# Performance work log

Measured on AMD Instinct MI355X. Metric: run time of the kernel, lower is better.

## Reference

```python
import jax, jax.numpy as jnp
import numpy as np

T_ENC = 80
MAX_LEN = 80
B = 64
D_IN = 4096
EU = 1024
DU = 1024
VOCAB = 20000
ATT = 80


def _lstm_scan(xs, h0, c0, W_ih, W_hh, b_ih, b_hh):
    """Single-layer LSTM over leading time dim. xs: [T,B,I]. Returns (ys[T,B,H], hT, cT)."""
    def step(carry, x):
        h, c = carry
        g = x @ W_ih.T + b_ih + h @ W_hh.T + b_hh
        i, f, gg, o = jnp.split(g, 4, axis=-1)
        c = jax.nn.sigmoid(f) * c + jax.nn.sigmoid(i) * jnp.tanh(gg)
        h = jax.nn.sigmoid(o) * jnp.tanh(c)
        return (h, c), h
    (hT, cT), ys = jax.lax.scan(step, (h0, c0), xs)
    return ys, hT, cT


def setup_inputs() -> dict:
    key = jax.random.key(0)
    ks = jax.random.split(key, 20)
    s = 0.05
    inp = {
        "input_data": jax.random.normal(ks[0], (T_ENC, B, D_IN), jnp.float32),
        "correct_answer": jax.random.normal(ks[1], (MAX_LEN, B, VOCAB), jnp.float32),
        # encoder LSTM params (torch gate order i,f,g,o)
        "enc_W_ih": jax.random.normal(ks[2], (4 * EU, D_IN), jnp.float32) * s,
        "enc_W_hh": jax.random.normal(ks[3], (4 * EU, EU), jnp.float32) * s,
        "enc_b_ih": jax.random.normal(ks[4], (4 * EU,), jnp.float32) * s,
        "enc_b_hh": jax.random.normal(ks[5], (4 * EU,), jnp.float32) * s,
        # decoder LSTM: input = decoder_unit + encoder_unit
        "dec_W_ih": jax.random.normal(ks[6], (4 * DU, DU + EU), jnp.float32) * s,
        "dec_W_hh": jax.random.normal(ks[7], (4 * DU, DU), jnp.float32) * s,
        "dec_b_ih": jax.random.normal(ks[8], (4 * DU,), jnp.float32) * s,
        "dec_b_hh": jax.random.normal(ks[9], (4 * DU,), jnp.float32) * s,
        # embeddings
        "in_emb_W": jax.random.normal(ks[10], (DU, VOCAB), jnp.float32) * s,
        "in_emb_b": jax.random.normal(ks[11], (DU,), jnp.float32) * s,
        "out_emb_W": jax.random.normal(ks[12], (VOCAB, DU), jnp.float32) * s,
        "out_emb_b": jax.random.normal(ks[13], (VOCAB,), jnp.float32) * s,
        # attention: linear_l1du_max ((d_l+1)*d_u -> 80), linear_2du_du (2*d_u -> d_u)
        "att_W1": jax.random.normal(ks[14], (ATT, 2 * DU), jnp.float32) * s,
        "att_b1": jax.random.normal(ks[15], (ATT,), jnp.float32) * s,
        "att_W2": jax.random.normal(ks[16], (DU, 2 * DU), jnp.float32) * s,
        "att_b2": jax.random.normal(ks[17], (DU,), jnp.float32) * s,
        "prelu_w": jnp.full((1,), 0.25, jnp.float32),  # PReLU(num_parameters=1) init
        "max_len": 80,
        "real_ans_length": jax.random.randint(ks[18], (B,), 0, 80),
    }
    return inp


def reference(input_data, correct_answer,
              enc_W_ih, enc_W_hh, enc_b_ih, enc_b_hh,
              dec_W_ih, dec_W_hh, dec_b_ih, dec_b_hh,
              in_emb_W, in_emb_b, out_emb_W, out_emb_b,
              att_W1, att_b1, att_W2, att_b2, prelu_w,
              max_len, real_ans_length):
    z_eh = jnp.zeros((B, EU), jnp.float32)
    z_dh = jnp.zeros((B, DU), jnp.float32)

    # encoding stage
    enc_seq, enc_h, enc_c = _lstm_scan(input_data, z_eh, z_eh, enc_W_ih, enc_W_hh, enc_b_ih, enc_b_hh)
    pad_tag = jnp.zeros((input_data.shape[0], B, DU), jnp.float32)
    dec_in0 = jnp.concatenate([enc_seq, pad_tag], axis=2)
    dec_out_seq, dec_h, dec_c = _lstm_scan(dec_in0, z_dh, z_dh, dec_W_ih, dec_W_hh, dec_b_ih, dec_b_hh)

    # encoder over zero padding inputs (continues encoder state)
    pad_in = jnp.zeros((max_len, B, D_IN), jnp.float32)
    enc_pad_seq, _, _ = _lstm_scan(pad_in, enc_h, enc_c, enc_W_ih, enc_W_hh, enc_b_ih, enc_b_hh)

    # teacher-forced samples (schedule_sample_rate == 1 -> always ground truth)
    bos = jnp.zeros((B, VOCAB), jnp.float32).at[:, -2].set(1.0)
    sample0 = bos @ in_emb_W.T + in_emb_b                              # [B, DU]
    samples_rest = correct_answer[1:max_len] @ in_emb_W.T + in_emb_b  # [max_len-1, B, DU]
    samples = jnp.concatenate([sample0[None], samples_rest], axis=0)   # [max_len, B, DU]

    E = enc_seq  # [80, B, EU]; attention weights have exactly 80 slots

    def dec_step(carry, inp):
        h, c = carry
        sample, enc_pad = inp
        # Attention: i = h (single layer), a = concat(i, word)
        a = jnp.concatenate([h, sample], axis=-1)          # [B, 2*DU]
        w = jax.nn.softmax(a @ att_W1.T + att_b1, axis=1)  # [B, 80]
        f = jnp.einsum('bs,sbh->bh', w, E)                 # [B, EU]
        cc = jnp.concatenate([sample, f], axis=-1)         # [B, 2*DU]
        z = cc @ att_W2.T + att_b2
        o = jnp.where(z >= 0, z, prelu_w[0] * z)           # PReLU (scalar param)
        context = o + enc_pad                              # [B, EU]
        x = jnp.concatenate([sample, context], axis=-1)    # [B, DU+EU]
        g = x @ dec_W_ih.T + dec_b_ih + h @ dec_W_hh.T + dec_b_hh
        gi, gf, gg, go = jnp.split(g, 4, axis=-1)
        c = jax.nn.sigmoid(gf) * c + jax.nn.sigmoid(gi) * jnp.tanh(gg)
        h = jax.nn.sigmoid(go) * jnp.tanh(c)
        word = h @ out_emb_W.T + out_emb_b                 # [B, VOCAB]
        return (h, c), word

    (_, _), words = jax.lax.scan(dec_step, (dec_h, dec_c), (samples, enc_pad_seq))
    return words  # [max_len, B, VOCAB]
```

## Files before the change

### kernel.cpp

```cpp
#include <hip/hip_runtime.h>
#include <cstddef>
#include <cstdint>

typedef __attribute__((ext_vector_type(8))) short short8v;
typedef __attribute__((ext_vector_type(4))) float f32x4;

__device__ __forceinline__ float sigmf(float x) { return 1.0f / (1.0f + __expf(-x)); }

__device__ __forceinline__ unsigned short bf16_rn(float x) {
    union { float f; unsigned u; } v; v.f = x;
    unsigned r = v.u + 0x7FFF + ((v.u >> 16) & 1);
    return (unsigned short)(r >> 16);
}
__device__ __forceinline__ float bf16_to_f(unsigned short h) {
    union { unsigned u; float f; } v; v.u = ((unsigned)h) << 16; return v.f;
}
__device__ __forceinline__ unsigned long long pack4(unsigned short a, unsigned short b,
                                                    unsigned short c, unsigned short d) {
    return (unsigned long long)a | ((unsigned long long)b << 16)
         | ((unsigned long long)c << 32) | ((unsigned long long)d << 48);
}

#define MFMA_(d, va, vb) d = __builtin_amdgcn_mfma_f32_16x16x32_bf16(va, vb, d, 0, 0, 0)

#define AT_LD(p)        __hip_atomic_load((p), __ATOMIC_RELAXED, __HIP_MEMORY_SCOPE_AGENT)
#define AT_ST(p, v)     __hip_atomic_store((p), (v), __ATOMIC_RELAXED, __HIP_MEMORY_SCOPE_AGENT)
#define AT_ST_REL(p, v) __hip_atomic_store((p), (v), __ATOMIC_RELEASE, __HIP_MEMORY_SCOPE_AGENT)
#define AT_ADD(p, v)    __hip_atomic_fetch_add((p), (v), __ATOMIC_RELAXED, __HIP_MEMORY_SCOPE_AGENT)

__device__ __forceinline__ void write_frag3_nt(unsigned short* __restrict__ dst, int NRGW,
                                               int r, int k, float x)
{
    unsigned short hi = bf16_rn(x); float r1 = x - bf16_to_f(hi);
    unsigned short md = bf16_rn(r1);
    unsigned short lo = bf16_rn(r1 - bf16_to_f(md));
    int base = (((r >> 4) * 32 + (k >> 5)) * 64 + ((k >> 3) & 3) * 16 + (r & 15)) * 8 + (k & 7);
    int ps = NRGW * 16384;
    __builtin_nontemporal_store(hi, &dst[base]);
    __builtin_nontemporal_store(md, &dst[ps + base]);
    __builtin_nontemporal_store(lo, &dst[2 * ps + base]);
}

__launch_bounds__(256)
__global__ void rearr_frag(const float* __restrict__ src, int ld, int c0,
                           unsigned short* __restrict__ dst, int R, int K)
{
    int idx = blockIdx.x * 256 + threadIdx.x;
    int kpr = K >> 3;
    if (idx >= R * kpr) return;
    int r = idx / kpr, k = (idx % kpr) * 8;
    int NRGW = R >> 4;
    const float* s = src + (size_t)r * ld + c0 + k;
    float4 v0 = *(const float4*)s, v1 = *(const float4*)(s + 4);
    float xs[8] = {v0.x, v0.y, v0.z, v0.w, v1.x, v1.y, v1.z, v1.w};
    unsigned short hi[8], md[8], lo[8];
#pragma unroll
    for (int e = 0; e < 8; ++e) {
        hi[e] = bf16_rn(xs[e]); float r1 = xs[e] - bf16_to_f(hi[e]);
        md[e] = bf16_rn(r1);
        lo[e] = bf16_rn(r1 - bf16_to_f(md[e]));
    }
    int base = (((r >> 4) * 32 + (k >> 5)) * 64 + ((k >> 3) & 3) * 16 + (r & 15)) * 8;
    size_t ps = (size_t)NRGW * 16384;
    *(unsigned long long*)&dst[base]          = pack4(hi[0], hi[1], hi[2], hi[3]);
    *(unsigned long long*)&dst[base + 4]      = pack4(hi[4], hi[5], hi[6], hi[7]);
    *(unsigned long long*)&dst[ps + base]     = pack4(md[0], md[1], md[2], md[3]);
    *(unsigned long long*)&dst[ps + base + 4] = pack4(md[4], md[5], md[6], md[7]);
    *(unsigned long long*)&dst[2*ps + base]     = pack4(lo[0], lo[1], lo[2], lo[3]);
    *(unsigned long long*)&dst[2*ps + base + 4] = pack4(lo[4], lo[5], lo[6], lo[7]);
}

__device__ __forceinline__ void tree_barrier(unsigned* bar, int gidx, int ng, int bpg)
{
    __syncthreads();
    if (threadIdx.x == 0) {
        unsigned* gcnt = bar + gidx * 32;
        unsigned* ggen = bar + gidx * 32 + 1;
        unsigned* rcnt = bar + ng * 32;
        unsigned* rgen = bar + ng * 32 + 1;
        __threadfence();
        unsigned mygen = AT_LD(ggen);
        unsigned prev = AT_ADD(gcnt, 1u);
        if (prev == (unsigned)(bpg - 1)) {
            AT_ST(gcnt, 0u);
            unsigned rg = AT_LD(rgen);
            unsigned rprev = AT_ADD(rcnt, 1u);
            if (rprev == (unsigned)(ng - 1)) {
                AT_ST(rcnt, 0u);
                AT_ST_REL(rgen, rg + 1u);
            } else {
                while (AT_LD(rgen) == rg) __builtin_amdgcn_s_sleep(1);
            }
            AT_ST_REL(ggen, mygen + 1u);
        } else {
            while (AT_LD(ggen) == mygen) __builtin_amdgcn_s_sleep(1);
        }
        __threadfence();
    }
    __syncthreads();
}

template <int NS>
__launch_bounds__(256, 2)
__global__ void gemm_mfma_split(const float* __restrict__ A, int lda,
                                const float* __restrict__ W, int ldw,
                                float* __restrict__ C, int ldc,
                                const float* __restrict__ bias,
                                int M, int N, int K)
{
    __shared__ unsigned short Abf[NS][128][40];
    __shared__ unsigned short Bbf[NS][128][40];
    const int tid = threadIdx.x;
    const int m0 = blockIdx.y * 128, n0 = blockIdx.x * 128;
    const int wave = tid >> 6, lane = tid & 63;
    const int wr = wave >> 1, wc = wave & 1;
    const int lr = lane & 15, lk = (lane >> 4) * 8;

    f32x4 acc[4][4];
#pragma unroll
    for (int i = 0; i < 4; ++i)
#pragma unroll
        for (int j = 0; j < 4; ++j) acc[i][j] = (f32x4){0.f, 0.f, 0.f, 0.f};

    const int arow = tid >> 1;
    const int akh  = (tid & 1) * 16;
    int gr = m0 + arow; if (gr > M - 1) gr = M - 1;
    int gn = n0 + arow; if (gn > N - 1) gn = N - 1;
    const float* aptr = A + (size_t)gr * lda + akh;
    const float* wptr = W + (size_t)gn * ldw + akh;

    for (int k0 = 0; k0 < K; k0 += 32) {
#pragma unroll
        for (int q = 0; q < 4; ++q) {
            float4 v = *(const float4*)(aptr + k0 + q * 4);
            float xs[4] = {v.x, v.y, v.z, v.w};
            unsigned short h[4], hm[4], hl[4];
#pragma unroll
            for (int e = 0; e < 4; ++e) {
                h[e] = bf16_rn(xs[e]);
                if (NS == 3) {
                    float r1 = xs[e] - bf16_to_f(h[e]);
                    hm[e] = bf16_rn(r1);
                    hl[e] = bf16_rn(r1 - bf16_to_f(hm[e]));
                }
            }
            *(unsigned long long*)&Abf[0][arow][akh + q * 4] = pack4(h[0], h[1], h[2], h[3]);
            if (NS == 3) {
                *(unsigned long long*)&Abf[1][arow][akh + q * 4] = pack4(hm[0], hm[1], hm[2], hm[3]);
                *(unsigned long long*)&Abf[2][arow][akh + q * 4] = pack4(hl[0], hl[1], hl[2], hl[3]);
            }
        }
#pragma unroll
        for (int q = 0; q < 4; ++q) {
            float4 v = *(const float4*)(wptr + k0 + q * 4);
            float xs[4] = {v.x, v.y, v.z, v.w};
            unsigned short h[4], hm[4], hl[4];
#pragma unroll
            for (int e = 0; e < 4; ++e) {
                h[e] = bf16_rn(xs[e]);
                if (NS == 3) {
                    float r1 = xs[e] - bf16_to_f(h[e]);
                    hm[e] = bf16_rn(r1);
                    hl[e] = bf16_rn(r1 - bf16_to_f(hm[e]));
                }
            }
            *(unsigned long long*)&Bbf[0][arow][akh + q * 4] = pack4(h[0], h[1], h[2], h[3]);
            if (NS == 3) {
                *(unsigned long long*)&Bbf[1][arow][akh + q * 4] = pack4(hm[0], hm[1], hm[2], hm[3]);
                *(unsigned long long*)&Bbf[2][arow][akh + q * 4] = pack4(hl[0], hl[1], hl[2], hl[3]);
            }
        }
        __syncthreads();

        short8v a[NS][4], b[4];
#pragma unroll
        for (int p = 0; p < NS; ++p)
#pragma unroll
            for (int i = 0; i < 4; ++i)
                a[p][i] = *(const short8v*)&Abf[p][wr * 64 + i * 16 + lr][lk];
#pragma unroll
        for (int q = 0; q < NS; ++q) {
#pragma unroll
            for (int j = 0; j < 4; ++j)
                b[j] = *(const short8v*)&Bbf[q][wc * 64 + j * 16 + lr][lk];
            const int pmax = (NS == 1) ? 1 : (3 - q);
#pragma unroll
            for (int p = 0; p < 3; ++p) {
                if (p >= pmax) break;
#pragma unroll
                for (int i = 0; i < 4; ++i)
#pragma unroll
                    for (int j = 0; j < 4; ++j)
                        acc[i][j] = __builtin_amdgcn_mfma_f32_16x16x32_bf16(
                            a[p][i], b[j], acc[i][j], 0, 0, 0);
            }
        }
        __syncthreads();
    }

    const int crow = (lane >> 4) * 4;
#pragma unroll
    for (int i = 0; i < 4; ++i) {
        int mbase = m0 + wr * 64 + i * 16 + crow;
#pragma unroll
        for (int j = 0; j < 4; ++j) {
            int n = n0 + wc * 64 + j * 16 + lr;
            if (n < N) {
                float bv = bias[n];
#pragma unroll
                for (int r = 0; r < 4; ++r) {
                    int m = mbase + r;
                    if (m < M) C[(size_t)m * ldc + n] = acc[i][j][r] + bv;
                }
            }
        }
    }
}

__launch_bounds__(256)
__global__ void zero_f(float* __restrict__ p, int n)
{
    int i = blockIdx.x * 256 + threadIdx.x;
    if (i < n) p[i] = 0.f;
}

__launch_bounds__(256)
__global__ void vec_add2(const float* __restrict__ a, const float* __restrict__ b,
                         float* __restrict__ o, int n)
{
    int i = blockIdx.x * 256 + threadIdx.x;
    if (i < n) o[i] = a[i] + b[i];
}

__launch_bounds__(256)
__global__ void sample0_fill(const float* __restrict__ emW, const float* __restrict__ emb,
                             float* __restrict__ samples)
{
    int idx = blockIdx.x * 256 + threadIdx.x;
    int d = idx & 1023;
    samples[idx] = emW[(size_t)d * 20000 + 19998] + emb[d];
}

__device__ __forceinline__ void stage_A(unsigned short* __restrict__ LDSA,
                                        const unsigned short* __restrict__ src,
                                        int rg, int tid)
{
#pragma unroll
    for (int p = 0; p < 3; ++p) {
        const unsigned short* sp = src + (size_t)(p * 4 + rg) * 16384;
        unsigned short* dp = LDSA + p * 16384;
#pragma unroll
        for (int it = 0; it < 4; ++it) {
            int idx = tid + it * 512;
            *(short8v*)&dp[idx * 8] = *(const short8v*)&sp[idx * 8];
        }
    }
}

__device__ __forceinline__ f32x4 mfma16(const unsigned short* __restrict__ LDSA,
                                        const short8v* __restrict__ wreg,
                                        int kh, int lane)
{
    f32x4 acc0 = (f32x4){0.f,0.f,0.f,0.f}, acc1 = acc0;
#pragma unroll
    for (int i = 0; i < 16; ++i) {
        int kf = kh * 16 + i;
        short8v a0 = *(const short8v*)&LDSA[(kf * 64 + lane) * 8];
        short8v a1 = *(const short8v*)&LDSA[16384 + (kf * 64 + lane) * 8];
        short8v a2 = *(const short8v*)&LDSA[32768 + (kf * 64 + lane) * 8];
        short8v b0 = wreg[i * 3 + 0], b1 = wreg[i * 3 + 1], b2 = wreg[i * 3 + 2];
        f32x4& A = (i & 1) ? acc1 : acc0;
        MFMA_(A, a0, b0); MFMA_(A, a0, b1); MFMA_(A, a1, b0);
        MFMA_(A, a1, b1); MFMA_(A, a0, b2); MFMA_(A, a2, b0);
    }
    return acc0 + acc1;
}

__launch_bounds__(512, 1)
__attribute__((amdgpu_waves_per_eu(1, 2)))
__global__ void coop_enc80(const unsigned short* __restrict__ WencF,
                           const float* __restrict__ Xbig,
                           unsigned short* __restrict__ hfrag,
                           float* __restrict__ enc_seq,
                           float* __restrict__ cglobE,
                           unsigned* __restrict__ bar)
{
    __shared__ unsigned short LDSA[3 * 16384];
    __shared__ float gbuf[8][16][16];
    const int bid = blockIdx.x, tid = threadIdx.x;
    const int w = tid >> 6, lane = tid & 63;
    const int g = w & 3, kh = w >> 2;
    const int rg = bid & 3, cg = bid >> 2;
    const int wbase = g * 64 + cg;
    const int r_l = (tid & 255) >> 4, c_l = tid & 15;
    const int row = rg * 16 + r_l, col = cg * 16 + c_l;
    float cstate = 0.f;

    short8v wreg[48];
#pragma unroll
    for (int i = 0; i < 16; ++i) {
        int kf = kh * 16 + i;
#pragma unroll
        for (int p = 0; p < 3; ++p)
            wreg[i * 3 + p] = *(const short8v*)&WencF[((size_t)(p * 256 + wbase) * 32 + kf) * 512 + lane * 8];
    }

    float pf[4];
    if (tid < 256) {
#pragma unroll
        for (int g2 = 0; g2 < 4; ++g2)
            pf[g2] = Xbig[(size_t)row * 4096 + g2 * 1024 + col];
    }

    for (int s = 0; s < 80; ++s) {
        const unsigned short* hf = hfrag + (s & 1) * 196608;
        stage_A(LDSA, hf, rg, tid);
        __syncthreads();
        f32x4 acc = mfma16(LDSA, wreg, kh, lane);
#pragma unroll
        for (int r = 0; r < 4; ++r)
            gbuf[w][(lane >> 4) * 4 + r][lane & 15] = acc[r];
        __syncthreads();

        if (tid < 256) {
            float gv[4];
#pragma unroll
            for (int g2 = 0; g2 < 4; ++g2)
                gv[g2] = gbuf[g2][r_l][c_l] + gbuf[4 + g2][r_l][c_l] + pf[g2];
            float cn = sigmf(gv[1]) * cstate + sigmf(gv[0]) * tanhf(gv[2]);
            float hn = sigmf(gv[3]) * tanhf(cn);
            cstate = cn;
            __builtin_nontemporal_store(hn, &enc_seq[(size_t)s * 65536 + row * 1024 + col]);
            write_frag3_nt(hfrag + ((s + 1) & 1) * 196608, 4, row, col, hn);
            if (s == 79) __builtin_nontemporal_store(cstate, &cglobE[row * 1024 + col]);
            else {
#pragma unroll
                for (int g2 = 0; g2 < 4; ++g2)
                    pf[g2] = Xbig[((size_t)(s + 1) * 64 + row) * 4096 + g2 * 1024 + col];
            }
        }
        tree_barrier(bar, bid >> 5, 8, 32);
    }
}

__launch_bounds__(512, 1)
__attribute__((amdgpu_waves_per_eu(1, 2)))
__global__ void coop_padwarm(const unsigned short* __restrict__ WencF,
                             const unsigned short* __restrict__ WdecF,
                             const float* __restrict__ benc,
                             const float* __restrict__ Xwarm,
                             const float* __restrict__ cglobE,
                             unsigned short* __restrict__ hfragE,
                             unsigned short* __restrict__ hfragD,
                             float* __restrict__ enc_pad,
                             float* __restrict__ cglobD,
                             float* __restrict__ h_fp32,
                             unsigned* __restrict__ barE,
                             unsigned* __restrict__ barW)
{
    __shared__ unsigned short LDSA[3 * 16384];
    __shared__ float gbuf[8][16][16];
    const int bid = blockIdx.x, tid = threadIdx.x;
    const int w = tid >> 6, lane = tid & 63;
    const int g = w & 3, kh = w >> 2;
    const bool isW = bid >= 128;
    const int lb = bid & 127;
    const int rg2 = lb & 1, cg = lb >> 1;
    const int wbase = g * 64 + cg;
    const int r_l = (tid & 255) >> 4, c_l = tid & 15;
    const int col = cg * 16 + c_l;
    const unsigned short* Wf = isW ? WdecF : WencF;
    unsigned short* hfrag = isW ? hfragD : hfragE;
    unsigned* bar = isW ? barW : barE;

    short8v wreg[48];
#pragma unroll
    for (int i = 0; i < 16; ++i) {
        int kf = kh * 16 + i;
#pragma unroll
        for (int p = 0; p < 3; ++p)
            wreg[i * 3 + p] = *(const short8v*)&Wf[((size_t)(p * 256 + wbase) * 32 + kf) * 512 + lane * 8];
    }

    float cst[2] = {0.f, 0.f};
    float pfx[2][4];
    if (tid < 256) {
#pragma unroll
        for (int l = 0; l < 2; ++l) {
            int row = rg2 * 32 + l * 16 + r_l;
            if (!isW) cst[l] = cglobE[row * 1024 + col];
#pragma unroll
            for (int g2 = 0; g2 < 4; ++g2)
                pfx[l][g2] = isW ? Xwarm[(size_t)row * 4096 + g2 * 1024 + col]
                                 : benc[g2 * 1024 + col];
        }
    }

    for (int s = 0; s < 80; ++s) {
        const unsigned short* hf = hfrag + (s & 1) * 196608;
        unsigned short* hout = hfrag + ((s + 1) & 1) * 196608;
#pragma unroll
        for (int l = 0; l < 2; ++l) {
            const int rgi = rg2 * 2 + l;
            stage_A(LDSA, hf, rgi, tid);
            __syncthreads();
            f32x4 acc = mfma16(LDSA, wreg, kh, lane);
#pragma unroll
            for (int r = 0; r < 4; ++r)
                gbuf[w][(lane >> 4) * 4 + r][lane & 15] = acc[r];
            __syncthreads();
            if (tid < 256) {
                const int row = rgi * 16 + r_l;
                float gv[4];
#pragma unroll
                for (int g2 = 0; g2 < 4; ++g2)
                    gv[g2] = gbuf[g2][r_l][c_l] + gbuf[4 + g2][r_l][c_l] + pfx[l][g2];
                float cn = sigmf(gv[1]) * cst[l] + sigmf(gv[0]) * tanhf(gv[2]);
                float hn = sigmf(gv[3]) * tanhf(cn);
                cst[l] = cn;
                if (!isW)
                    __builtin_nontemporal_store(hn, &enc_pad[(size_t)s * 65536 + row * 1024 + col]);
                write_frag3_nt(hout, 4, row, col, hn);
                if (isW) {
                    if (s == 79) {
                        __builtin_nontemporal_store(hn, &h_fp32[row * 1024 + col]);
                        __builtin_nontemporal_store(cn, &cglobD[row * 1024 + col]);
                    } else {
#pragma unroll
                        for (int g2 = 0; g2 < 4; ++g2)
                            pfx[l][g2] = Xwarm[((size_t)(s + 1) * 64 + row) * 4096 + g2 * 1024 + col];
                    }
                }
            }
            __syncthreads();
        }
        tree_barrier(bar, (lb >> 5), 4, 32);
    }
}

__launch_bounds__(512, 2)
__global__ void coop_dec80(const unsigned short* __restrict__ WihcF,
                           const unsigned short* __restrict__ WhhF,
                           const float* __restrict__ W1,
                           const float* __restrict__ EW2,
                           const float* __restrict__ S_g,
                           const float* __restrict__ ctxS,
                           const float* __restrict__ S_log,
                           const float* __restrict__ enc_pad,
                           const float* __restrict__ prelu_w,
                           const float* __restrict__ h_fp32,
                           const float* __restrict__ cglobD,
                           unsigned short* __restrict__ hfrag,
                           unsigned short* __restrict__ ctxfrag,
                           float* __restrict__ plog,
                           float* __restrict__ h_all,
                           float* __restrict__ gsum,
                           unsigned* __restrict__ bar)
{
    __shared__ float EW2T[80 * 256];
    __shared__ float gred[8][1024];
    __shared__ float hq[256];
    __shared__ float wsm[80];
    __shared__ float rbuf[128];
    const int bid = blockIdx.x, tid = threadIdx.x;
    const int w = tid >> 6, lane = tid & 63;
    const int gg = bid >> 6, cg = bid & 63;
    const int wbase = gg * 64 + cg;
    const int kq = w;
    const int b = bid >> 2, jc = bid & 3;
    const float pw = prelu_w[0];

    const unsigned short* Wsrc = (kq < 4) ? WihcF : WhhF;
    const int kfbase = (kq & 3) * 8;
    short8v wreg[24];
#pragma unroll
    for (int i = 0; i < 8; ++i) {
#pragma unroll
        for (int p = 0; p < 3; ++p)
            wreg[i * 3 + p] = *(const short8v*)&Wsrc[((size_t)(p * 256 + wbase) * 32 + kfbase + i) * 512 + lane * 8];
    }

    float cstate = (tid < 256) ? cglobD[b * 1024 + jc * 256 + tid] : 0.f;

    for (int i = tid; i < 80 * 256; i += 512) {
        int ss = i >> 8, j = i & 255;
        EW2T[i] = EW2[((size_t)ss * 64 + b) * 1024 + jc * 256 + j];
    }
    __syncthreads();

    for (int s = 80; s < 160; ++s) {
        unsigned short* hout = hfrag + ((s + 1) & 1) * 196608;
        const unsigned short* hf = hfrag + (s & 1) * 196608;
        const int t = s - 80;

        if (s == 80) {
            float* hsm_ = (float*)gred;
            for (int i = tid; i < 1024; i += 512) hsm_[i] = h_fp32[b * 1024 + i];
            __syncthreads();
#pragma unroll
            for (int i = 0; i < 10; ++i) {
                int sx = w * 10 + i;
                float p = 0.f;
#pragma unroll
                for (int q = 0; q < 16; ++q)
                    p = fmaf(hsm_[lane + q * 64], W1[(size_t)sx * 2048 + lane + q * 64], p);
#pragma unroll
                for (int off = 32; off; off >>= 1) p += __shfl_down(p, off, 64);
                if (lane == 0) wsm[sx] = p + S_log[((size_t)t * 64 + b) * 80 + sx];
            }
            __syncthreads();
        } else {
            if (tid < 80) {
                float l4 = plog[(b * 4 + 0) * 80 + tid] + plog[(b * 4 + 1) * 80 + tid]
                         + plog[(b * 4 + 2) * 80 + tid] + plog[(b * 4 + 3) * 80 + tid];
                wsm[tid] = l4 + S_log[((size_t)t * 64 + b) * 80 + tid];
            }
            __syncthreads();
        }
        float v = (tid < 80) ? wsm[tid] : -3.4e38f;
        if (tid < 128) rbuf[tid] = v;
        __syncthreads();
        for (int off = 64; off >= 1; off >>= 1) {
            if (tid < off) rbuf[tid] = fmaxf(rbuf[tid], rbuf[tid + off]);
            __syncthreads();
        }
        float mx = rbuf[0];
        __syncthreads();
        float e = (tid < 80) ? __expf(wsm[tid] - mx) : 0.f;
        if (tid < 128) rbuf[tid] = e;
        __syncthreads();
        for (int off = 64; off >= 1; off >>= 1) {
            if (tid < off) rbuf[tid] += rbuf[tid + off];
            __syncthreads();
        }
        float inv = 1.f / rbuf[0];
        __syncthreads();
        if (tid < 80) wsm[tid] = e * inv;
        __syncthreads();
        if (tid < 256) {
            float f = 0.f;
#pragma unroll 8
            for (int ss = 0; ss < 80; ++ss)
                f = fmaf(wsm[ss], EW2T[ss * 256 + tid], f);
            int col = jc * 256 + tid;
            float val = f + ctxS[((size_t)t * 64 + b) * 1024 + col];
            val = (val >= 0.f) ? val : pw * val;
            val += enc_pad[((size_t)t * 64 + b) * 1024 + col];
            write_frag3_nt(ctxfrag, 4, b, col, val);
        }
        tree_barrier(bar, bid >> 5, 8, 32);

        float pf[4];
        if (tid < 256) {
            const float* xb = S_g + ((size_t)t * 64 + b) * 4096;
            int col = jc * 256 + tid;
#pragma unroll
            for (int g2 = 0; g2 < 4; ++g2) pf[g2] = xb[g2 * 1024 + col];
        }

        {
            f32x4 acc[4];
#pragma unroll
            for (int rg = 0; rg < 4; ++rg) acc[rg] = (f32x4){0.f,0.f,0.f,0.f};
            const unsigned short* asrc = (kq < 4) ? ctxfrag : hf;
#pragma unroll
            for (int i = 0; i < 8; ++i) {
                int kfl = kfbase + i;
#pragma unroll
                for (int rg = 0; rg < 4; ++rg) {
                    const unsigned short* ab = asrc + ((size_t)rg * 32 + kfl) * 512 + lane * 8;
                    short8v a0 = *(const short8v*)&ab[0];
                    short8v a1 = *(const short8v*)&ab[65536];
                    short8v a2 = *(const short8v*)&ab[131072];
                    short8v b0 = wreg[i * 3 + 0], b1 = wreg[i * 3 + 1], b2 = wreg[i * 3 + 2];
                    MFMA_(acc[rg], a0, b0); MFMA_(acc[rg], a0, b1); MFMA_(acc[rg], a1, b0);
                    MFMA_(acc[rg], a1, b1); MFMA_(acc[rg], a0, b2); MFMA_(acc[rg], a2, b0);
                }
            }
#pragma unroll
            for (int rg = 0; rg < 4; ++rg)
#pragma unroll
                for (int r = 0; r < 4; ++r)
                    gred[w][rg * 256 + lane * 4 + r] = acc[rg][r];
            __syncthreads();
#pragma unroll
            for (int e2 = 0; e2 < 2; ++e2) {
                int slot = tid * 2 + e2;
                int rg = slot >> 8, l = (slot >> 2) & 63, r = slot & 3;
                float sum = 0.f;
#pragma unroll
                for (int w2 = 0; w2 < 8; ++w2) sum += gred[w2][slot];
                int row = rg * 16 + (l >> 4) * 4 + r;
                int col = cg * 16 + (l & 15);
                __builtin_nontemporal_store(sum, &gsum[((size_t)gg * 64 + row) * 1024 + col]);
            }
        }
        tree_barrier(bar, bid >> 5, 8, 32);

        if (tid < 256) {
            int col = jc * 256 + tid;
            float gv[4];
#pragma unroll
            for (int g2 = 0; g2 < 4; ++g2)
                gv[g2] = gsum[((size_t)g2 * 64 + b) * 1024 + col] + pf[g2];
            float cn = sigmf(gv[1]) * cstate + sigmf(gv[0]) * tanhf(gv[2]);
            float hn = sigmf(gv[3]) * tanhf(cn);
            cstate = cn;
            __builtin_nontemporal_store(hn, &h_all[((size_t)t * 64 + b) * 1024 + col]);
            write_frag3_nt(hout, 4, b, col, hn);
            hq[tid] = hn;
        }
        __syncthreads();
        if (s < 159) {
#pragma unroll
            for (int i = 0; i < 10; ++i) {
                int sx = w * 10 + i;
                float p = 0.f;
#pragma unroll
                for (int q = 0; q < 4; ++q)
                    p = fmaf(hq[lane + q * 64], W1[(size_t)sx * 2048 + jc * 256 + lane + q * 64], p);
#pragma unroll
                for (int off = 32; off; off >>= 1) p += __shfl_down(p, off, 64);
                if (lane == 0) __builtin_nontemporal_store(p, &plog[(b * 4 + jc) * 80 + sx]);
            }
        }
        tree_barrier(bar, bid >> 5, 8, 32);
    }
}

extern "C" void kernel_launch(void* const* d_in, const int* in_sizes, int n_in,
                              void* d_out, int out_size, void* d_ws, size_t ws_size,
                              hipStream_t stream)
{
    (void)in_sizes; (void)n_in; (void)out_size; (void)ws_size;

    const float* input_data     = (const float*)d_in[0];
    const float* correct_answer = (const float*)d_in[1];
    const float* enc_W_ih = (const float*)d_in[2];
    const float* enc_W_hh = (const float*)d_in[3];
    const float* enc_b_ih = (const float*)d_in[4];
    const float* enc_b_hh = (const float*)d_in[5];
    const float* dec_W_ih = (const float*)d_in[6];
    const float* dec_W_hh = (const float*)d_in[7];
    const float* dec_b_ih = (const float*)d_in[8];
    const float* dec_b_hh = (const float*)d_in[9];
    const float* in_emb_W = (const float*)d_in[10];
    const float* in_emb_b = (const float*)d_in[11];
    const float* out_emb_W = (const float*)d_in[12];
    const float* out_emb_b = (const float*)d_in[13];
    const float* att_W1 = (const float*)d_in[14];
    const float* att_b1 = (const float*)d_in[15];
    const float* att_W2 = (const float*)d_in[16];
    const float* att_b2 = (const float*)d_in[17];
    const float* prelu_w = (const float*)d_in[18];

    float* out = (float*)d_out;
    char* ws = (char*)d_ws;

    float* Xbig    = out;
    float* S_g     = out + 20971520;
    float* ctxS    = out + 41943040;
    float* S_log   = out + 47185920;
    float* samples = out + 47595520;
    float* EW2     = out + 52838400;
    unsigned short* WencF = (unsigned short*)(out + 58081280);
    unsigned short* WhhDF = (unsigned short*)(out + 64372736);
    unsigned short* WihcF = (unsigned short*)(out + 70664192);

    size_t off = 0;
    auto alloc = [&](size_t nfloats) { float* p = (float*)(ws + off); off += nfloats * 4; return p; };
    float* enc_seq = alloc(80 * 64 * 1024);
    float* enc_pad = alloc(80 * 64 * 1024);
    float* h_all   = alloc(80 * 64 * 1024);
    float* benc    = alloc(4096);
    float* bdec    = alloc(4096);
    float* zb      = alloc(1024);
    float* hfragE_f = alloc(196608);
    float* hfragD_f = alloc(196608);
    float* ctxfrag_f= alloc(98304);
    float* plog     = alloc(64 * 4 * 80);
    float* gsum     = alloc(262144);
    float* cglobE   = alloc(65536);
    float* cglobD   = alloc(65536);
    float* h_fp32   = alloc(65536);
    float* bar_f    = alloc(2048);
    unsigned short* hfragE  = (unsigned short*)hfragE_f;
    unsigned short* hfragD  = (unsigned short*)hfragD_f;
    unsigned short* ctxfrag = (unsigned short*)ctxfrag_f;
    unsigned* barE1 = (unsigned*)bar_f;
    unsigned* barPE = ((unsigned*)bar_f) + 512;
    unsigned* barPW = ((unsigned*)bar_f) + 1024;
    unsigned* barD  = ((unsigned*)bar_f) + 1536;

    auto big3 = [&](const float* A, int lda, const float* W, int ldw,
                    float* C, int ldc, const float* bias, int M, int N, int K) {
        dim3 g((N + 127) / 128, (M + 127) / 128);
        hipLaunchKernelGGL((gemm_mfma_split<3>), g, dim3(256), 0, stream,
                           A, lda, W, ldw, C, ldc, bias, M, N, K);
    };

    hipLaunchKernelGGL(vec_add2, dim3(16), dim3(256), 0, stream, enc_b_ih, enc_b_hh, benc, 4096);
    hipLaunchKernelGGL(vec_add2, dim3(16), dim3(256), 0, stream, dec_b_ih, dec_b_hh, bdec, 4096);
    hipLaunchKernelGGL(zero_f, dim3(4), dim3(256), 0, stream, zb, 1024);
    hipLaunchKernelGGL(zero_f, dim3(768), dim3(256), 0, stream, hfragE_f, 196608);
    hipLaunchKernelGGL(zero_f, dim3(768), dim3(256), 0, stream, hfragD_f, 196608);
    hipLaunchKernelGGL(zero_f, dim3(8), dim3(256), 0, stream, bar_f, 2048);

    hipLaunchKernelGGL(rearr_frag, dim3(2048), dim3(256), 0, stream, enc_W_hh, 1024, 0, WencF, 4096, 1024);
    hipLaunchKernelGGL(rearr_frag, dim3(2048), dim3(256), 0, stream, dec_W_hh, 1024, 0, WhhDF, 4096, 1024);
    hipLaunchKernelGGL(rearr_frag, dim3(2048), dim3(256), 0, stream, dec_W_ih, 2048, 1024, WihcF, 4096, 1024);

    big3(input_data, 4096, enc_W_ih, 4096, Xbig, 4096, benc, 5120, 4096, 4096);
    hipLaunchKernelGGL(sample0_fill, dim3(256), dim3(256), 0, stream, in_emb_W, in_emb_b, samples);
    big3(correct_answer + (size_t)64 * 20000, 20000, in_emb_W, 20000,
         samples + 65536, 1024, in_emb_b, 5056, 1024, 20000);
    big3(samples, 1024, dec_W_ih, 2048, S_g, 4096, bdec, 5120, 4096, 1024);
    big3(samples, 1024, att_W2, 2048, ctxS, 1024, att_b2, 5120, 1024, 1024);
    big3(samples, 1024, att_W1 + 1024, 2048, S_log, 80, att_b1, 5120, 80, 1024);

    hipLaunchKernelGGL(coop_enc80, dim3(256), dim3(512), 0, stream,
                       WencF, Xbig, hfragE, enc_seq, cglobE, barE1);

    big3(enc_seq, 1024, dec_W_ih, 2048, Xbig, 4096, bdec, 5120, 4096, 1024);
    big3(enc_seq, 1024, att_W2 + 1024, 2048, EW2, 1024, zb, 5120, 1024, 1024);

    hipLaunchKernelGGL(coop_padwarm, dim3(256), dim3(512), 0, stream,
                       WencF, WhhDF, benc, Xbig, cglobE,
                       hfragE, hfragD, enc_pad, cglobD, h_fp32, barPE, barPW);

    hipLaunchKernelGGL(coop_dec80, dim3(256), dim3(512), 0, stream,
                       WihcF, WhhDF, att_W1, EW2, S_g, ctxS, S_log,
                       enc_pad, prelu_w, h_fp32, cglobD,
                       hfragD, ctxfrag, plog, h_all, gsum, barD);

    {
        dim3 g((20000 + 127) / 128, (5120 + 127) / 128);
        hipLaunchKernelGGL((gemm_mfma_split<1>), g, dim3(256), 0, stream,
                           h_all, 1024, out_emb_W, 1024, out, 20000, out_emb_b, 5120, 20000, 1024);
    }
}
```

Baseline: 14.67 ms.

## Compute full LSTM row redundantly per block to drop a grid barrier per decoder step

Every block now computes the LSTM cell update for all 1024 columns of its batch row, keeping the full cell state in registers and the full h in shared memory. It then computes the attention logits, softmax and context for the next step locally, without exchanging partial logits through global memory. This removes the plog exchange and one grid-wide tree barrier per decoder step. The cost is fourfold redundant gate math and W1 dot products in every block, plus more global reads of gsum and S_g per block.

```diff
diff --git a/kernel.cpp b/kernel.cpp
--- a/kernel.cpp
+++ b/kernel.cpp
@@ -452,14 +452,13 @@
                            const float* __restrict__ cglobD,
                            unsigned short* __restrict__ hfrag,
                            unsigned short* __restrict__ ctxfrag,
-                           float* __restrict__ plog,
                            float* __restrict__ h_all,
                            float* __restrict__ gsum,
                            unsigned* __restrict__ bar)
 {
     __shared__ float EW2T[80 * 256];
     __shared__ float gred[8][1024];
-    __shared__ float hq[256];
+    __shared__ float hfull[1024];
     __shared__ float wsm[80];
     __shared__ float rbuf[128];
     const int bid = blockIdx.x, tid = threadIdx.x;
@@ -480,43 +479,30 @@
             wreg[i * 3 + p] = *(const short8v*)&Wsrc[((size_t)(p * 256 + wbase) * 32 + kfbase + i) * 512 + lane * 8];
     }
 
-    float cstate = (tid < 256) ? cglobD[b * 1024 + jc * 256 + tid] : 0.f;
+    float c2[2];
+    c2[0] = cglobD[b * 1024 + tid * 2];
+    c2[1] = cglobD[b * 1024 + tid * 2 + 1];
 
     for (int i = tid; i < 80 * 256; i += 512) {
         int ss = i >> 8, j = i & 255;
         EW2T[i] = EW2[((size_t)ss * 64 + b) * 1024 + jc * 256 + j];
     }
+
+    for (int i = tid; i < 1024; i += 512) hfull[i] = h_fp32[b * 1024 + i];
     __syncthreads();
-
-    for (int s = 80; s < 160; ++s) {
-        unsigned short* hout = hfrag + ((s + 1) & 1) * 196608;
-        const unsigned short* hf = hfrag + (s & 1) * 196608;
-        const int t = s - 80;
-
-        if (s == 80) {
-            float* hsm_ = (float*)gred;
-            for (int i = tid; i < 1024; i += 512) hsm_[i] = h_fp32[b * 1024 + i];
-            __syncthreads();
-#pragma unroll
-            for (int i = 0; i < 10; ++i) {
-                int sx = w * 10 + i;
-                float p = 0.f;
-#pragma unroll
-                for (int q = 0; q < 16; ++q)
-                    p = fmaf(hsm_[lane + q * 64], W1[(size_t)sx * 2048 + lane + q * 64], p);
-#pragma unroll
-                for (int off = 32; off; off >>= 1) p += __shfl_down(p, off, 64);
-                if (lane == 0) wsm[sx] = p + S_log[((size_t)t * 64 + b) * 80 + sx];
-            }
-            __syncthreads();
-        } else {
-            if (tid < 80) {
-                float l4 = plog[(b * 4 + 0) * 80 + tid] + plog[(b * 4 + 1) * 80 + tid]
-                         + plog[(b * 4 + 2) * 80 + tid] + plog[(b * 4 + 3) * 80 + tid];
-                wsm[tid] = l4 + S_log[((size_t)t * 64 + b) * 80 + tid];
-            }
-            __syncthreads();
-        }
+    {
+#pragma unroll
+        for (int i = 0; i < 10; ++i) {
+            int sx = w * 10 + i;
+            float p = 0.f;
+#pragma unroll
+            for (int q = 0; q < 16; ++q)
+                p = fmaf(hfull[lane + q * 64], W1[(size_t)sx * 2048 + lane + q * 64], p);
+#pragma unroll
+            for (int off = 32; off; off >>= 1) p += __shfl_down(p, off, 64);
+            if (lane == 0) wsm[sx] = p + S_log[(size_t)b * 80 + sx];
+        }
+        __syncthreads();
         float v = (tid < 80) ? wsm[tid] : -3.4e38f;
         if (tid < 128) rbuf[tid] = v;
         __syncthreads();
@@ -543,19 +529,28 @@
             for (int ss = 0; ss < 80; ++ss)
                 f = fmaf(wsm[ss], EW2T[ss * 256 + tid], f);
             int col = jc * 256 + tid;
-            float val = f + ctxS[((size_t)t * 64 + b) * 1024 + col];
+            float val = f + ctxS[(size_t)b * 1024 + col];
             val = (val >= 0.f) ? val : pw * val;
-            val += enc_pad[((size_t)t * 64 + b) * 1024 + col];
+            val += enc_pad[(size_t)b * 1024 + col];
             write_frag3_nt(ctxfrag, 4, b, col, val);
         }
-        tree_barrier(bar, bid >> 5, 8, 32);
-
-        float pf[4];
-        if (tid < 256) {
+    }
+    tree_barrier(bar, bid >> 5, 8, 32);
+
+    for (int t = 0; t < 80; ++t) {
+        const int s = 80 + t;
+        unsigned short* hout = hfrag + ((s + 1) & 1) * 196608;
+        const unsigned short* hf = hfrag + (s & 1) * 196608;
+
+        float pf2[2][4];
+        {
             const float* xb = S_g + ((size_t)t * 64 + b) * 4096;
-            int col = jc * 256 + tid;
-#pragma unroll
-            for (int g2 = 0; g2 < 4; ++g2) pf[g2] = xb[g2 * 1024 + col];
+#pragma unroll
+            for (int e = 0; e < 2; ++e) {
+                int col = tid * 2 + e;
+#pragma unroll
+                for (int g2 = 0; g2 < 4; ++g2) pf2[e][g2] = xb[g2 * 1024 + col];
+            }
         }
 
         {
@@ -597,31 +592,74 @@
         }
         tree_barrier(bar, bid >> 5, 8, 32);
 
-        if (tid < 256) {
-            int col = jc * 256 + tid;
-            float gv[4];
-#pragma unroll
-            for (int g2 = 0; g2 < 4; ++g2)
-                gv[g2] = gsum[((size_t)g2 * 64 + b) * 1024 + col] + pf[g2];
-            float cn = sigmf(gv[1]) * cstate + sigmf(gv[0]) * tanhf(gv[2]);
-            float hn = sigmf(gv[3]) * tanhf(cn);
-            cstate = cn;
-            __builtin_nontemporal_store(hn, &h_all[((size_t)t * 64 + b) * 1024 + col]);
-            write_frag3_nt(hout, 4, b, col, hn);
-            hq[tid] = hn;
-        }
-        __syncthreads();
-        if (s < 159) {
-#pragma unroll
-            for (int i = 0; i < 10; ++i) {
-                int sx = w * 10 + i;
-                float p = 0.f;
-#pragma unroll
-                for (int q = 0; q < 4; ++q)
-                    p = fmaf(hq[lane + q * 64], W1[(size_t)sx * 2048 + jc * 256 + lane + q * 64], p);
-#pragma unroll
-                for (int off = 32; off; off >>= 1) p += __shfl_down(p, off, 64);
-                if (lane == 0) __builtin_nontemporal_store(p, &plog[(b * 4 + jc) * 80 + sx]);
+        {
+            float hv[2];
+#pragma unroll
+            for (int e = 0; e < 2; ++e) {
+                int col = tid * 2 + e;
+                float gv[4];
+#pragma unroll
+                for (int g2 = 0; g2 < 4; ++g2)
+                    gv[g2] = gsum[((size_t)g2 * 64 + b) * 1024 + col] + pf2[e][g2];
+                float cn = sigmf(gv[1]) * c2[e] + sigmf(gv[0]) * tanhf(gv[2]);
+                float hn = sigmf(gv[3]) * tanhf(cn);
+                c2[e] = cn;
+                hfull[col] = hn;
+                hv[e] = hn;
+            }
+            __syncthreads();
+            if (tid >= jc * 128 && tid < (jc + 1) * 128) {
+#pragma unroll
+                for (int e = 0; e < 2; ++e) {
+                    int col = tid * 2 + e;
+                    __builtin_nontemporal_store(hv[e], &h_all[((size_t)t * 64 + b) * 1024 + col]);
+                    write_frag3_nt(hout, 4, b, col, hv[e]);
+                }
+            }
+            if (t < 79) {
+#pragma unroll
+                for (int i = 0; i < 10; ++i) {
+                    int sx = w * 10 + i;
+                    float p = 0.f;
+#pragma unroll
+                    for (int q = 0; q < 16; ++q)
+                        p = fmaf(hfull[lane + q * 64], W1[(size_t)sx * 2048 + lane + q * 64], p);
+#pragma unroll
+                    for (int off = 32; off; off >>= 1) p += __shfl_down(p, off, 64);
+                    if (lane == 0) wsm[sx] = p + S_log[((size_t)(t + 1) * 64 + b) * 80 + sx];
+                }
+                __syncthreads();
+                float v = (tid < 80) ? wsm[tid] : -3.4e38f;
+                if (tid < 128) rbuf[tid] = v;
+                __syncthreads();
+                for (int off = 64; off >= 1; off >>= 1) {
+                    if (tid < off) rbuf[tid] = fmaxf(rbuf[tid], rbuf[tid + off]);
+                    __syncthreads();
+                }
+                float mx = rbuf[0];
+                __syncthreads();
+                float e = (tid < 80) ? __expf(wsm[tid] - mx) : 0.f;
+                if (tid < 128) rbuf[tid] = e;
+                __syncthreads();
+                for (int off = 64; off >= 1; off >>= 1) {
+                    if (tid < off) rbuf[tid] += rbuf[tid + off];
+                    __syncthreads();
+                }
+                float inv = 1.f / rbuf[0];
+                __syncthreads();
+                if (tid < 80) wsm[tid] = e * inv;
+                __syncthreads();
+                if (tid < 256) {
+                    float f = 0.f;
+#pragma unroll 8
+                    for (int ss = 0; ss < 80; ++ss)
+                        f = fmaf(wsm[ss], EW2T[ss * 256 + tid], f);
+                    int col = jc * 256 + tid;
+                    float val = f + ctxS[((size_t)(t + 1) * 64 + b) * 1024 + col];
+                    val = (val >= 0.f) ? val : pw * val;
+                    val += enc_pad[((size_t)(t + 1) * 64 + b) * 1024 + col];
+                    write_frag3_nt(ctxfrag, 4, b, col, val);
+                }
             }
         }
         tree_barrier(bar, bid >> 5, 8, 32);
@@ -678,7 +716,6 @@
     float* hfragE_f = alloc(196608);
     float* hfragD_f = alloc(196608);
     float* ctxfrag_f= alloc(98304);
-    float* plog     = alloc(64 * 4 * 80);
     float* gsum     = alloc(262144);
     float* cglobE   = alloc(65536);
     float* cglobD   = alloc(65536);
@@ -731,7 +768,7 @@
     hipLaunchKernelGGL(coop_dec80, dim3(256), dim3(512), 0, stream,
                        WihcF, WhhDF, att_W1, EW2, S_g, ctxS, S_log,
                        enc_pad, prelu_w, h_fp32, cglobD,
-                       hfragD, ctxfrag, plog, h_all, gsum, barD);
+                       hfragD, ctxfrag, h_all, gsum, barD);
 
     {
         dim3 g((20000 + 127) / 128, (5120 + 127) / 128);
```

New measurement: 13.83 ms (median of 2 runs). -5.7%, faster.
